# Kernel optimization log

Measured on AMD Instinct MI355X. Metric: run time of the kernel, lower is better.

The kernel has to match this reference:

```python
import jax, jax.numpy as jnp
import numpy as np

B, S, D = 16, 1024, 1024
HEADS = 16
DIM_HEAD = D // HEADS  # 64, used only for the softmax scale (no head split in source)
EPS = 1e-6


def setup_inputs() -> dict:
    key = jax.random.key(0)
    ks = jax.random.split(key, 18)
    inp = {}
    names = ['q_real', 'q_imag', 'k_real', 'k_imag', 'v_real', 'v_imag']
    for i, n in enumerate(names):
        inp[n] = jax.random.normal(ks[i], (B, S, D), dtype=jnp.float32)
    wnames = ['Wq_r', 'Wq_i', 'Wk_r', 'Wk_i', 'Wv_r', 'Wv_i']
    for i, n in enumerate(wnames):
        inp[n] = jax.random.normal(ks[6 + i], (D, D), dtype=jnp.float32) * 0.02
        inp['b' + n[1:]] = jax.random.normal(ks[12 + (i % 6)], (D,), dtype=jnp.float32) * 0.02
    inp['a_2'] = jnp.ones((D,), dtype=jnp.float32)
    inp['b_2'] = jnp.ones((D,), dtype=jnp.float32)
    return inp


def reference(q_real, q_imag, k_real, k_imag, v_real, v_imag,
              Wq_r, bq_r, Wq_i, bq_i, Wk_r, bk_r, Wk_i, bk_i,
              Wv_r, bv_r, Wv_i, bv_i, a_2, b_2):
    # torch nn.Linear: y = x @ W.T + b
    qr = q_real @ Wq_r.T + bq_r
    qi = q_imag @ Wq_i.T + bq_i
    kr = k_real @ Wk_r.T + bk_r
    ki = k_imag @ Wk_i.T + bk_i
    vr = v_real @ Wv_r.T + bv_r
    vi = v_imag @ Wv_i.T + bv_i
    # Faithful to source: transpose(-2, 1) on a 3D tensor is a no-op, so the
    # real branch contracts q's feature dim with k's *sequence* dim (S == D).
    scores = (jnp.einsum('bsd,bde->bse', qr, kr)
              + jnp.einsum('bsd,btd->bst', qi, ki)) / jnp.sqrt(jnp.float32(DIM_HEAD))
    attn = jax.nn.softmax(scores, axis=-1)  # [B, S, S]
    out_r = attn @ vr  # [B, S, D]
    out_i = attn @ vi
    z = out_r + 1j * out_i  # complex64
    # Complex LayerNorm: mean/var computed in complex arithmetic (not |.|^2)
    mean = jnp.mean(z, axis=-1, keepdims=True)
    var = jnp.mean((z - mean) ** 2, axis=-1, keepdims=True)
    std = jnp.sqrt(var + EPS)  # complex sqrt
    y = a_2 * ((z - mean) / std) + b_2
    return jnp.stack([y.real, y.imag])  # [2, B, S, D] real view of complex output
```

## Files before the change

### kernel.cpp

```cpp
#include <hip/hip_runtime.h>


#define MB 1048576L

typedef _Float16 h8 __attribute__((ext_vector_type(8)));
typedef _Float16 h4 __attribute__((ext_vector_type(4)));
typedef float f32x16 __attribute__((ext_vector_type(16)));

__device__ __forceinline__ float wave_sum(float x) {
#pragma unroll
  for (int o = 32; o; o >>= 1) x += __shfl_xor(x, o);
  return x;
}
__device__ __forceinline__ float wave_max(float x) {
#pragma unroll
  for (int o = 32; o; o >>= 1) x = fmaxf(x, __shfl_xor(x, o));
  return x;
}

__device__ __forceinline__ void async16(const char* g, char* l) {
  __builtin_amdgcn_global_load_lds(
      (const __attribute__((address_space(1))) unsigned int*)g,
      (__attribute__((address_space(3))) unsigned int*)l, 16, 0, 0);
}

__device__ __forceinline__ void split8(const float* v, h8& hi, h8& lo) {
#pragma unroll
  for (int j = 0; j < 8; ++j) {
    _Float16 h = (_Float16)v[j];
    hi[j] = h;
    lo[j] = (_Float16)(v[j] - (float)h);
  }
}

__global__ void split_pass(const float* __restrict__ in, char* __restrict__ out, long n8) {
  long i = (long)blockIdx.x * blockDim.x + threadIdx.x;
  if (i >= n8) return;
  float v[8];
  const float4* p = (const float4*)(in + i * 8);
  float4 a = p[0], b = p[1];
  v[0] = a.x; v[1] = a.y; v[2] = a.z; v[3] = a.w;
  v[4] = b.x; v[5] = b.y; v[6] = b.z; v[7] = b.w;
  h8 hi, lo;
  split8(v, hi, lo);
  *(h8*)(out + i * 32) = hi;
  *(h8*)(out + i * 32 + 16) = lo;
}

template <int EPI>
__launch_bounds__(256, 3)
__global__ void gemm_sp(const char* __restrict__ A1, const char* __restrict__ B1,
                        const char* __restrict__ A2, const char* __restrict__ B2,
                        int npair, const float* __restrict__ bias,
                        float* __restrict__ Cf, char* __restrict__ Ct,
                        float scale, long zA, long zB, long zC) {
  __shared__ __align__(16) char lds[32768];
  const int tid = threadIdx.x;
  const int wid = tid >> 6, lane = tid & 63;
  const int ln31 = lane & 31, half = lane >> 5;
  const int bm0 = blockIdx.y * 128, bn0 = blockIdx.x * 128;
  const long z = blockIdx.z;

  const char* Ap[2] = {A1 + z * zA, A2 ? A2 + z * zA : nullptr};
  const char* Bp[2] = {B1 + z * zB, B2 ? B2 + z * zB : nullptr};

  const int srow = lane >> 3;
  const int sunit = (lane & 7) ^ srow;
  char* ldsA = lds + wid * 4096;
  char* ldsB = lds + 16384 + wid * 4096;

  const int e = ln31 & 7;
  const int rowA0 = ((wid >> 1) * 64 + ln31) * 128;
  const int rowB0 = 16384 + ((wid & 1) * 64 + ln31) * 128;
  int uoff[2][2];
#pragma unroll
  for (int ks = 0; ks < 2; ++ks)
#pragma unroll
    for (int c = 0; c < 2; ++c) uoff[ks][c] = ((4 * ks + 2 * half + c) ^ e) * 16;

  f32x16 acc[2][2] = {};

  for (int p = 0; p < npair; ++p) {
    const char* a0 = Ap[p] + (long)(bm0 + wid * 32 + srow) * 4096 + sunit * 16;
    const char* b0 = Bp[p] + (long)(bn0 + wid * 32 + srow) * 4096 + sunit * 16;
    for (int chunk = 0; chunk < 32; ++chunk) {
      __syncthreads();
#pragma unroll
      for (int i = 0; i < 4; ++i) async16(a0 + i * 32768, ldsA + i * 1024);
#pragma unroll
      for (int i = 0; i < 4; ++i) async16(b0 + i * 32768, ldsB + i * 1024);
      __syncthreads();
#pragma unroll
      for (int ks = 0; ks < 2; ++ks) {
        h8 ah[2], al[2], bh[2], bl[2];
#pragma unroll
        for (int mt = 0; mt < 2; ++mt) {
          ah[mt] = *(const h8*)(lds + rowA0 + mt * 4096 + uoff[ks][0]);
          al[mt] = *(const h8*)(lds + rowA0 + mt * 4096 + uoff[ks][1]);
        }
#pragma unroll
        for (int nt = 0; nt < 2; ++nt) {
          bh[nt] = *(const h8*)(lds + rowB0 + nt * 4096 + uoff[ks][0]);
          bl[nt] = *(const h8*)(lds + rowB0 + nt * 4096 + uoff[ks][1]);
        }
#pragma unroll
        for (int mt = 0; mt < 2; ++mt)
#pragma unroll
          for (int nt = 0; nt < 2; ++nt) {
            acc[mt][nt] = __builtin_amdgcn_mfma_f32_32x32x16_f16(ah[mt], bh[nt], acc[mt][nt], 0, 0, 0);
            acc[mt][nt] = __builtin_amdgcn_mfma_f32_32x32x16_f16(ah[mt], bl[nt], acc[mt][nt], 0, 0, 0);
            acc[mt][nt] = __builtin_amdgcn_mfma_f32_32x32x16_f16(al[mt], bh[nt], acc[mt][nt], 0, 0, 0);
          }
      }
      a0 += 128;
      b0 += 128;
    }
  }

  const int wm0 = (wid >> 1) * 64, wn0 = (wid & 1) * 64;
  if (EPI == 0) {
    float* C = Cf + z * zC;
#pragma unroll
    for (int nt = 0; nt < 2; ++nt) {
      const int col = bn0 + wn0 + nt * 32 + ln31;
      const float bv = bias ? bias[col] : 0.0f;
#pragma unroll
      for (int mt = 0; mt < 2; ++mt) {
#pragma unroll
        for (int q = 0; q < 4; ++q) {
#pragma unroll
          for (int i = 0; i < 4; ++i) {
            const int row = bm0 + wm0 + mt * 32 + q * 8 + half * 4 + i;
            C[(long)row * 1024 + col] = acc[mt][nt][q * 4 + i] * scale + bv;
          }
        }
      }
    }
  } else {
    const long b = bm0 >> 10;
    char* Tb = Ct + b * (4 * MB);
    const int sbase = bm0 & 1023;
#pragma unroll
    for (int nt = 0; nt < 2; ++nt) {
      const int n = bn0 + wn0 + nt * 32 + ln31;
      const float bv = bias ? bias[n] : 0.0f;
#pragma unroll
      for (int mt = 0; mt < 2; ++mt) {
#pragma unroll
        for (int q = 0; q < 4; ++q) {
          const int sl = sbase + wm0 + mt * 32 + q * 8 + half * 4;
          h4 hv, lv;
#pragma unroll
          for (int i = 0; i < 4; ++i) {
            float y = acc[mt][nt][q * 4 + i] * scale + bv;
            _Float16 h = (_Float16)y;
            hv[i] = h;
            lv[i] = (_Float16)(y - (float)h);
          }
          char* dst = Tb + (long)n * 4096 + (sl >> 3) * 32 + (sl & 7) * 2;
          *(h4*)dst = hv;
          *(h4*)(dst + 16) = lv;
        }
      }
    }
  }
}

__launch_bounds__(128)
__global__ void softmax_split(const float* __restrict__ S, char* __restrict__ attn) {
  const long row = blockIdx.x;
  const int t = threadIdx.x;
  const float* p = S + row * 1024 + t * 8;
  float4 a = *(const float4*)p, b = *(const float4*)(p + 4);
  float v[8] = {a.x, a.y, a.z, a.w, b.x, b.y, b.z, b.w};
  float m = v[0];
#pragma unroll
  for (int j = 1; j < 8; ++j) m = fmaxf(m, v[j]);
  m = wave_max(m);
  __shared__ float redm[2], reds[2];
  const int wave = t >> 6, lane = t & 63;
  if (lane == 0) redm[wave] = m;
  __syncthreads();
  m = fmaxf(redm[0], redm[1]);
  float s = 0.f;
#pragma unroll
  for (int j = 0; j < 8; ++j) {
    v[j] = __expf(v[j] - m);
    s += v[j];
  }
  s = wave_sum(s);
  if (lane == 0) reds[wave] = s;
  __syncthreads();
  const float inv = 1.0f / (reds[0] + reds[1]);
#pragma unroll
  for (int j = 0; j < 8; ++j) v[j] *= inv;
  h8 hi, lo;
  split8(v, hi, lo);
  char* dst = attn + row * 4096 + t * 32;
  *(h8*)dst = hi;
  *(h8*)(dst + 16) = lo;
}

__launch_bounds__(256)
__global__ void complex_ln(const float* __restrict__ inr, const float* __restrict__ ini,
                           float* __restrict__ outr, float* __restrict__ outi,
                           const float* __restrict__ a2, const float* __restrict__ b2) {
  const long row = blockIdx.x;
  const int tid = threadIdx.x;
  const float* xr = inr + row * 1024;
  const float* xi = ini + row * 1024;
  float4 r4 = *(const float4*)(xr + tid * 4);
  float4 i4 = *(const float4*)(xi + tid * 4);
  float sx = r4.x + r4.y + r4.z + r4.w;
  float sy = i4.x + i4.y + i4.z + i4.w;
  float sxx = r4.x * r4.x + r4.y * r4.y + r4.z * r4.z + r4.w * r4.w;
  float syy = i4.x * i4.x + i4.y * i4.y + i4.z * i4.z + i4.w * i4.w;
  float sxy = r4.x * i4.x + r4.y * i4.y + r4.z * i4.z + r4.w * i4.w;
  sx = wave_sum(sx); sy = wave_sum(sy);
  sxx = wave_sum(sxx); syy = wave_sum(syy); sxy = wave_sum(sxy);
  __shared__ float red[4][5];
  const int wave = tid >> 6, lane = tid & 63;
  if (lane == 0) {
    red[wave][0] = sx; red[wave][1] = sy; red[wave][2] = sxx;
    red[wave][3] = syy; red[wave][4] = sxy;
  }
  __syncthreads();
  sx = red[0][0] + red[1][0] + red[2][0] + red[3][0];
  sy = red[0][1] + red[1][1] + red[2][1] + red[3][1];
  sxx = red[0][2] + red[1][2] + red[2][2] + red[3][2];
  syy = red[0][3] + red[1][3] + red[2][3] + red[3][3];
  sxy = red[0][4] + red[1][4] + red[2][4] + red[3][4];
  const float invN = 1.0f / 1024.0f;
  const float mx = sx * invN, my = sy * invN;
  const float vx = (sxx * invN - mx * mx) - (syy * invN - my * my);
  const float vy = 2.0f * (sxy * invN - mx * my);
  const float wx = vx + 1e-6f, wy = vy;
  const float rm = sqrtf(wx * wx + wy * wy);
  const float sre = sqrtf(fmaxf(rm + wx, 0.0f) * 0.5f);
  const float sim = copysignf(sqrtf(fmaxf(rm - wx, 0.0f) * 0.5f), wy);
  const float ir = 1.0f / fmaxf(rm, 1e-30f);
  float4 a4 = *(const float4*)(a2 + tid * 4);
  float4 b4 = *(const float4*)(b2 + tid * 4);
  float4 orr, oii;
  {
    float zx = r4.x - mx, zy = i4.x - my;
    orr.x = a4.x * ((zx * sre + zy * sim) * ir) + b4.x;
    oii.x = a4.x * ((zy * sre - zx * sim) * ir);
  }
  {
    float zx = r4.y - mx, zy = i4.y - my;
    orr.y = a4.y * ((zx * sre + zy * sim) * ir) + b4.y;
    oii.y = a4.y * ((zy * sre - zx * sim) * ir);
  }
  {
    float zx = r4.z - mx, zy = i4.z - my;
    orr.z = a4.z * ((zx * sre + zy * sim) * ir) + b4.z;
    oii.z = a4.z * ((zy * sre - zx * sim) * ir);
  }
  {
    float zx = r4.w - mx, zy = i4.w - my;
    orr.w = a4.w * ((zx * sre + zy * sim) * ir) + b4.w;
    oii.w = a4.w * ((zy * sre - zx * sim) * ir);
  }
  *(float4*)(outr + row * 1024 + tid * 4) = orr;
  *(float4*)(outi + row * 1024 + tid * 4) = oii;
}

extern "C" void kernel_launch(void* const* d_in, const int* in_sizes, int n_in,
                              void* d_out, int out_size, void* d_ws, size_t ws_size,
                              hipStream_t stream) {
  const float* X[6];
  for (int i = 0; i < 6; ++i) X[i] = (const float*)d_in[i];
  const float* W[6];
  const float* bia[6];
  for (int i = 0; i < 6; ++i) {
    W[i] = (const float*)d_in[6 + 2 * i];
    bia[i] = (const float*)d_in[7 + 2 * i];
  }
  const float* a2 = (const float*)d_in[18];
  const float* b2 = (const float*)d_in[19];

  char* ws = (char*)d_ws;
  char* qr = ws;
  char* qi = ws + 64 * MB;
  char* ki = ws + 128 * MB;
  char* krT = ws + 192 * MB;
  char* vrT = ws + 256 * MB;
  char* viT = ws + 320 * MB;
  char* Wsp[6];
  for (int i = 0; i < 6; ++i) Wsp[i] = ws + 384 * MB + (long)i * 4 * MB;

  char* dob = (char*)d_out;
  char* Xsp = dob;
  float* F0 = (float*)(dob + 64 * MB);
  float* Sf = (float*)dob;
  char* attn = dob + 64 * MB;
  float* outr = (float*)ws;
  float* outi = (float*)(ws + 64 * MB);

  dim3 blk(256);
  dim3 proj_g(8, 128, 1), bat_g(8, 8, 16);

  for (int i = 0; i < 6; ++i)
    split_pass<<<dim3(512), blk, 0, stream>>>(W[i], Wsp[i], 131072L);

  split_pass<<<dim3(8192), blk, 0, stream>>>(X[0], Xsp, 2097152L);
  gemm_sp<0><<<proj_g, blk, 0, stream>>>(Xsp, Wsp[0], nullptr, nullptr, 1, bia[0], F0, nullptr, 1.0f, 0, 0, 0);
  split_pass<<<dim3(8192), blk, 0, stream>>>(F0, qr, 2097152L);
  split_pass<<<dim3(8192), blk, 0, stream>>>(X[1], Xsp, 2097152L);
  gemm_sp<0><<<proj_g, blk, 0, stream>>>(Xsp, Wsp[1], nullptr, nullptr, 1, bia[1], F0, nullptr, 1.0f, 0, 0, 0);
  split_pass<<<dim3(8192), blk, 0, stream>>>(F0, qi, 2097152L);
  split_pass<<<dim3(8192), blk, 0, stream>>>(X[3], Xsp, 2097152L);
  gemm_sp<0><<<proj_g, blk, 0, stream>>>(Xsp, Wsp[3], nullptr, nullptr, 1, bia[3], F0, nullptr, 1.0f, 0, 0, 0);
  split_pass<<<dim3(8192), blk, 0, stream>>>(F0, ki, 2097152L);
  split_pass<<<dim3(8192), blk, 0, stream>>>(X[2], Xsp, 2097152L);
  gemm_sp<1><<<proj_g, blk, 0, stream>>>(Xsp, Wsp[2], nullptr, nullptr, 1, bia[2], nullptr, krT, 1.0f, 0, 0, 0);
  split_pass<<<dim3(8192), blk, 0, stream>>>(X[4], Xsp, 2097152L);
  gemm_sp<1><<<proj_g, blk, 0, stream>>>(Xsp, Wsp[4], nullptr, nullptr, 1, bia[4], nullptr, vrT, 1.0f, 0, 0, 0);
  split_pass<<<dim3(8192), blk, 0, stream>>>(X[5], Xsp, 2097152L);
  gemm_sp<1><<<proj_g, blk, 0, stream>>>(Xsp, Wsp[5], nullptr, nullptr, 1, bia[5], nullptr, viT, 1.0f, 0, 0, 0);

  gemm_sp<0><<<bat_g, blk, 0, stream>>>(qr, krT, qi, ki, 2, nullptr, Sf, nullptr, 0.125f,
                                        4 * MB, 4 * MB, 1048576L);
  softmax_split<<<dim3(16384), dim3(128), 0, stream>>>(Sf, attn);
  gemm_sp<0><<<bat_g, blk, 0, stream>>>(attn, vrT, nullptr, nullptr, 1, nullptr, outr, nullptr, 1.0f,
                                        4 * MB, 4 * MB, 1048576L);
  gemm_sp<0><<<bat_g, blk, 0, stream>>>(attn, viT, nullptr, nullptr, 1, nullptr, outi, nullptr, 1.0f,
                                        4 * MB, 4 * MB, 1048576L);
  complex_ln<<<dim3(16384), blk, 0, stream>>>(outr, outi, (float*)d_out,
                                              (float*)(dob + 64 * MB), a2, b2);
}
```

Measured before the change: 1.866 ms.

## Rewrite split-fp16 GEMM with 256x256 tiles and 4-stage async LDS pipeline

The GEMM kernel moves from 128x128 tiles with 256 threads and a single-buffered load/sync/compute loop to 256x256 tiles with 512 threads. A 4-deep ring of LDS buffers is filled by async global-to-LDS loads three steps ahead, with explicit vmcnt waits. It also narrows K steps to 64 bytes with a new swizzle and raises wave priority around the MFMA block. This is meant to hide global memory latency and raise arithmetic intensity per block. In exchange it uses 128KB of LDS per block, which cuts occupancy and leaves fewer blocks in the smaller grids.

Result: faster. 1.700 ms (-8.9%).

```diff
diff --git a/kernel.cpp b/kernel.cpp
--- a/kernel.cpp
+++ b/kernel.cpp
@@ -48,89 +48,110 @@
 }
 
 template <int EPI>
-__launch_bounds__(256, 3)
+__launch_bounds__(512, 2)
 __global__ void gemm_sp(const char* __restrict__ A1, const char* __restrict__ B1,
                         const char* __restrict__ A2, const char* __restrict__ B2,
                         int npair, const float* __restrict__ bias,
                         float* __restrict__ Cf, char* __restrict__ Ct,
                         float scale, long zA, long zB, long zC) {
-  __shared__ __align__(16) char lds[32768];
+  __shared__ __align__(16) char lds[131072];
   const int tid = threadIdx.x;
-  const int wid = tid >> 6, lane = tid & 63;
-  const int ln31 = lane & 31, half = lane >> 5;
-  const int bm0 = blockIdx.y * 128, bn0 = blockIdx.x * 128;
+  const int w = tid >> 6, lam = tid & 63;
+  const int ln31 = lam & 31, half = lam >> 5;
+  const int wr = w >> 2, wc = w & 3;
+  const int bm0 = blockIdx.y * 256, bn0 = blockIdx.x * 256;
   const long z = blockIdx.z;
 
-  const char* Ap[2] = {A1 + z * zA, A2 ? A2 + z * zA : nullptr};
-  const char* Bp[2] = {B1 + z * zB, B2 ? B2 + z * zB : nullptr};
-
-  const int srow = lane >> 3;
-  const int sunit = (lane & 7) ^ srow;
-  char* ldsA = lds + wid * 4096;
-  char* ldsB = lds + 16384 + wid * 4096;
-
-  const int e = ln31 & 7;
-  const int rowA0 = ((wid >> 1) * 64 + ln31) * 128;
-  const int rowB0 = 16384 + ((wid & 1) * 64 + ln31) * 128;
-  int uoff[2][2];
-#pragma unroll
-  for (int ks = 0; ks < 2; ++ks)
-#pragma unroll
-    for (int c = 0; c < 2; ++c) uoff[ks][c] = ((4 * ks + 2 * half + c) ^ e) * 16;
-
-  f32x16 acc[2][2] = {};
-
-  for (int p = 0; p < npair; ++p) {
-    const char* a0 = Ap[p] + (long)(bm0 + wid * 32 + srow) * 4096 + sunit * 16;
-    const char* b0 = Bp[p] + (long)(bn0 + wid * 32 + srow) * 4096 + sunit * 16;
-    for (int chunk = 0; chunk < 32; ++chunk) {
-      __syncthreads();
-#pragma unroll
-      for (int i = 0; i < 4; ++i) async16(a0 + i * 32768, ldsA + i * 1024);
-#pragma unroll
-      for (int i = 0; i < 4; ++i) async16(b0 + i * 32768, ldsB + i * 1024);
-      __syncthreads();
-#pragma unroll
-      for (int ks = 0; ks < 2; ++ks) {
-        h8 ah[2], al[2], bh[2], bl[2];
-#pragma unroll
-        for (int mt = 0; mt < 2; ++mt) {
-          ah[mt] = *(const h8*)(lds + rowA0 + mt * 4096 + uoff[ks][0]);
-          al[mt] = *(const h8*)(lds + rowA0 + mt * 4096 + uoff[ks][1]);
-        }
-#pragma unroll
-        for (int nt = 0; nt < 2; ++nt) {
-          bh[nt] = *(const h8*)(lds + rowB0 + nt * 4096 + uoff[ks][0]);
-          bl[nt] = *(const h8*)(lds + rowB0 + nt * 4096 + uoff[ks][1]);
-        }
-#pragma unroll
-        for (int mt = 0; mt < 2; ++mt)
-#pragma unroll
-          for (int nt = 0; nt < 2; ++nt) {
-            acc[mt][nt] = __builtin_amdgcn_mfma_f32_32x32x16_f16(ah[mt], bh[nt], acc[mt][nt], 0, 0, 0);
-            acc[mt][nt] = __builtin_amdgcn_mfma_f32_32x32x16_f16(ah[mt], bl[nt], acc[mt][nt], 0, 0, 0);
-            acc[mt][nt] = __builtin_amdgcn_mfma_f32_32x32x16_f16(al[mt], bh[nt], acc[mt][nt], 0, 0, 0);
-          }
+  const char* A1z = A1 + z * zA;
+  const char* B1z = B1 + z * zB;
+  const char* A2z = A2 ? A2 + z * zA : A1z;
+  const char* B2z = B2 ? B2 + z * zB : B1z;
+
+  const int stRow = w * 32 + (lam >> 2);
+  const int stU = (lam & 3) ^ ((lam >> 3) & 3);
+  const long sAo = (long)(bm0 + stRow) * 4096 + stU * 16;
+  const long sBo = (long)(bn0 + stRow) * 4096 + stU * 16;
+
+  const int e2 = (ln31 >> 1) & 3;
+  const int offH = ((2 * half) ^ e2) * 16;
+  const int offL = ((2 * half + 1) ^ e2) * 16;
+  const int rA = (wr * 128 + ln31) * 64;
+  const int rB = 16384 + (wc * 64 + ln31) * 64;
+
+  const int Nk = npair * 64;
+  f32x16 acc[4][2] = {};
+
+  auto STAGE = [&](int tt) {
+    const long ko = (long)(tt & 63) * 64;
+    char* d = lds + (tt & 3) * 32768 + w * 2048;
+    const char* As = ((tt >> 6) ? A2z : A1z) + sAo + ko;
+    const char* Bs = ((tt >> 6) ? B2z : B1z) + sBo + ko;
+    async16(As, d);
+    async16(As + 65536, d + 1024);
+    async16(Bs, d + 16384);
+    async16(Bs + 65536, d + 17408);
+  };
+
+  STAGE(0);
+  STAGE(1);
+  STAGE(2);
+  __builtin_amdgcn_sched_barrier(0);
+
+  for (int t = 0; t < Nk; ++t) {
+    const int left = Nk - t;
+    if (left > 3) STAGE(t + 3);
+    __builtin_amdgcn_sched_barrier(0);
+    if (left > 3)
+      asm volatile("s_waitcnt vmcnt(12)" ::: "memory");
+    else if (left == 3)
+      asm volatile("s_waitcnt vmcnt(8)" ::: "memory");
+    else if (left == 2)
+      asm volatile("s_waitcnt vmcnt(4)" ::: "memory");
+    else
+      asm volatile("s_waitcnt vmcnt(0)" ::: "memory");
+    __builtin_amdgcn_s_barrier();
+    __builtin_amdgcn_sched_barrier(0);
+
+    const char* bq = lds + (t & 3) * 32768;
+    h8 bh[2], bl[2], ah[4], al[4];
+#pragma unroll
+    for (int nt = 0; nt < 2; ++nt) {
+      bh[nt] = *(const h8*)(bq + rB + nt * 2048 + offH);
+      bl[nt] = *(const h8*)(bq + rB + nt * 2048 + offL);
+    }
+#pragma unroll
+    for (int mt = 0; mt < 4; ++mt) {
+      ah[mt] = *(const h8*)(bq + rA + mt * 2048 + offH);
+      al[mt] = *(const h8*)(bq + rA + mt * 2048 + offL);
+    }
+    __builtin_amdgcn_s_setprio(1);
+#pragma unroll
+    for (int mt = 0; mt < 4; ++mt)
+#pragma unroll
+      for (int nt = 0; nt < 2; ++nt) {
+        acc[mt][nt] = __builtin_amdgcn_mfma_f32_32x32x16_f16(ah[mt], bh[nt], acc[mt][nt], 0, 0, 0);
+        acc[mt][nt] = __builtin_amdgcn_mfma_f32_32x32x16_f16(ah[mt], bl[nt], acc[mt][nt], 0, 0, 0);
+        acc[mt][nt] = __builtin_amdgcn_mfma_f32_32x32x16_f16(al[mt], bh[nt], acc[mt][nt], 0, 0, 0);
       }
-      a0 += 128;
-      b0 += 128;
-    }
-  }
-
-  const int wm0 = (wid >> 1) * 64, wn0 = (wid & 1) * 64;
+    __builtin_amdgcn_s_setprio(0);
+    __builtin_amdgcn_sched_barrier(0);
+    __builtin_amdgcn_s_barrier();
+  }
+
+  const int wm = wr * 128, wn = wc * 64;
   if (EPI == 0) {
     float* C = Cf + z * zC;
 #pragma unroll
     for (int nt = 0; nt < 2; ++nt) {
-      const int col = bn0 + wn0 + nt * 32 + ln31;
+      const int col = bn0 + wn + nt * 32 + ln31;
       const float bv = bias ? bias[col] : 0.0f;
 #pragma unroll
-      for (int mt = 0; mt < 2; ++mt) {
+      for (int mt = 0; mt < 4; ++mt) {
 #pragma unroll
         for (int q = 0; q < 4; ++q) {
 #pragma unroll
           for (int i = 0; i < 4; ++i) {
-            const int row = bm0 + wm0 + mt * 32 + q * 8 + half * 4 + i;
+            const int row = bm0 + wm + mt * 32 + q * 8 + half * 4 + i;
             C[(long)row * 1024 + col] = acc[mt][nt][q * 4 + i] * scale + bv;
           }
         }
@@ -142,13 +163,13 @@
     const int sbase = bm0 & 1023;
 #pragma unroll
     for (int nt = 0; nt < 2; ++nt) {
-      const int n = bn0 + wn0 + nt * 32 + ln31;
+      const int n = bn0 + wn + nt * 32 + ln31;
       const float bv = bias ? bias[n] : 0.0f;
 #pragma unroll
-      for (int mt = 0; mt < 2; ++mt) {
+      for (int mt = 0; mt < 4; ++mt) {
 #pragma unroll
         for (int q = 0; q < 4; ++q) {
-          const int sl = sbase + wm0 + mt * 32 + q * 8 + half * 4;
+          const int sl = sbase + wm + mt * 32 + q * 8 + half * 4;
           h4 hv, lv;
 #pragma unroll
           for (int i = 0; i < 4; ++i) {
@@ -298,35 +319,35 @@
   float* outr = (float*)ws;
   float* outi = (float*)(ws + 64 * MB);
 
-  dim3 blk(256);
-  dim3 proj_g(8, 128, 1), bat_g(8, 8, 16);
+  dim3 blk(256), gblk(512);
+  dim3 proj_g(4, 64, 1), bat_g(4, 4, 16);
 
   for (int i = 0; i < 6; ++i)
     split_pass<<<dim3(512), blk, 0, stream>>>(W[i], Wsp[i], 131072L);
 
   split_pass<<<dim3(8192), blk, 0, stream>>>(X[0], Xsp, 2097152L);
-  gemm_sp<0><<<proj_g, blk, 0, stream>>>(Xsp, Wsp[0], nullptr, nullptr, 1, bia[0], F0, nullptr, 1.0f, 0, 0, 0);
+  gemm_sp<0><<<proj_g, gblk, 0, stream>>>(Xsp, Wsp[0], nullptr, nullptr, 1, bia[0], F0, nullptr, 1.0f, 0, 0, 0);
   split_pass<<<dim3(8192), blk, 0, stream>>>(F0, qr, 2097152L);
   split_pass<<<dim3(8192), blk, 0, stream>>>(X[1], Xsp, 2097152L);
-  gemm_sp<0><<<proj_g, blk, 0, stream>>>(Xsp, Wsp[1], nullptr, nullptr, 1, bia[1], F0, nullptr, 1.0f, 0, 0, 0);
+  gemm_sp<0><<<proj_g, gblk, 0, stream>>>(Xsp, Wsp[1], nullptr, nullptr, 1, bia[1], F0, nullptr, 1.0f, 0, 0, 0);
   split_pass<<<dim3(8192), blk, 0, stream>>>(F0, qi, 2097152L);
   split_pass<<<dim3(8192), blk, 0, stream>>>(X[3], Xsp, 2097152L);
-  gemm_sp<0><<<proj_g, blk, 0, stream>>>(Xsp, Wsp[3], nullptr, nullptr, 1, bia[3], F0, nullptr, 1.0f, 0, 0, 0);
+  gemm_sp<0><<<proj_g, gblk, 0, stream>>>(Xsp, Wsp[3], nullptr, nullptr, 1, bia[3], F0, nullptr, 1.0f, 0, 0, 0);
   split_pass<<<dim3(8192), blk, 0, stream>>>(F0, ki, 2097152L);
   split_pass<<<dim3(8192), blk, 0, stream>>>(X[2], Xsp, 2097152L);
-  gemm_sp<1><<<proj_g, blk, 0, stream>>>(Xsp, Wsp[2], nullptr, nullptr, 1, bia[2], nullptr, krT, 1.0f, 0, 0, 0);
+  gemm_sp<1><<<proj_g, gblk, 0, stream>>>(Xsp, Wsp[2], nullptr, nullptr, 1, bia[2], nullptr, krT, 1.0f, 0, 0, 0);
   split_pass<<<dim3(8192), blk, 0, stream>>>(X[4], Xsp, 2097152L);
-  gemm_sp<1><<<proj_g, blk, 0, stream>>>(Xsp, Wsp[4], nullptr, nullptr, 1, bia[4], nullptr, vrT, 1.0f, 0, 0, 0);
+  gemm_sp<1><<<proj_g, gblk, 0, stream>>>(Xsp, Wsp[4], nullptr, nullptr, 1, bia[4], nullptr, vrT, 1.0f, 0, 0, 0);
   split_pass<<<dim3(8192), blk, 0, stream>>>(X[5], Xsp, 2097152L);
-  gemm_sp<1><<<proj_g, blk, 0, stream>>>(Xsp, Wsp[5], nullptr, nullptr, 1, bia[5], nullptr, viT, 1.0f, 0, 0, 0);
-
-  gemm_sp<0><<<bat_g, blk, 0, stream>>>(qr, krT, qi, ki, 2, nullptr, Sf, nullptr, 0.125f,
-                                        4 * MB, 4 * MB, 1048576L);
+  gemm_sp<1><<<proj_g, gblk, 0, stream>>>(Xsp, Wsp[5], nullptr, nullptr, 1, bia[5], nullptr, viT, 1.0f, 0, 0, 0);
+
+  gemm_sp<0><<<bat_g, gblk, 0, stream>>>(qr, krT, qi, ki, 2, nullptr, Sf, nullptr, 0.125f,
+                                         4 * MB, 4 * MB, 1048576L);
   softmax_split<<<dim3(16384), dim3(128), 0, stream>>>(Sf, attn);
-  gemm_sp<0><<<bat_g, blk, 0, stream>>>(attn, vrT, nullptr, nullptr, 1, nullptr, outr, nullptr, 1.0f,
-                                        4 * MB, 4 * MB, 1048576L);
-  gemm_sp<0><<<bat_g, blk, 0, stream>>>(attn, viT, nullptr, nullptr, 1, nullptr, outi, nullptr, 1.0f,
-                                        4 * MB, 4 * MB, 1048576L);
+  gemm_sp<0><<<bat_g, gblk, 0, stream>>>(attn, vrT, nullptr, nullptr, 1, nullptr, outr, nullptr, 1.0f,
+                                         4 * MB, 4 * MB, 1048576L);
+  gemm_sp<0><<<bat_g, gblk, 0, stream>>>(attn, viT, nullptr, nullptr, 1, nullptr, outi, nullptr, 1.0f,
+                                         4 * MB, 4 * MB, 1048576L);
   complex_ln<<<dim3(16384), blk, 0, stream>>>(outr, outi, (float*)d_out,
                                               (float*)(dob + 64 * MB), a2, b2);
 }
```
